# Kernel optimization log

Hardware: AMD Instinct MI355X
Metric: run time of the kernel (lower is better)

The kernel has to match this reference:

```python
import jax, jax.numpy as jnp
import numpy as np

B, T, D, H = 4, 2048, 2048, 16
DH = D // H

def setup_inputs() -> dict:
    key = jax.random.key(0)
    ks = jax.random.split(key, 9)
    s = 1.0 / np.sqrt(D)
    return {
        "x": jax.random.normal(ks[0], (B, T, D), dtype=jnp.float32),
        "Wq": jax.random.uniform(ks[1], (D, D), jnp.float32, -s, s),
        "bq": jax.random.uniform(ks[2], (D,), jnp.float32, -s, s),
        "Wk": jax.random.uniform(ks[3], (D, D), jnp.float32, -s, s),
        "bk": jax.random.uniform(ks[4], (D,), jnp.float32, -s, s),
        "Wv": jax.random.uniform(ks[5], (D, D), jnp.float32, -s, s),
        "bv": jax.random.uniform(ks[6], (D,), jnp.float32, -s, s),
        "Wo": jax.random.uniform(ks[7], (D, D), jnp.float32, -s, s),
        "bo": jax.random.uniform(ks[8], (D,), jnp.float32, -s, s),
    }

def reference(x, Wq, bq, Wk, bk, Wv, bv, Wo, bo):
    # projections: [B,T,D] -> [B,H,T,DH]
    def split_heads(y):
        return y.reshape(B, T, H, DH).transpose(0, 2, 1, 3)
    q = split_heads(x @ Wq + bq)
    k = split_heads(x @ Wk + bk)
    v = split_heads(x @ Wv + bv)
    scale = DH ** -0.5
    scores = jnp.einsum('bhtd,bhsd->bhts', q, k) * scale  # [B,H,T,T]
    causal = jnp.tril(jnp.ones((T, T), dtype=bool))
    scores = jnp.where(causal[None, None], scores, -jnp.inf)
    weights = jax.nn.softmax(scores, axis=-1)
    out = jnp.einsum('bhts,bhsd->bhtd', weights, v)  # [B,H,T,DH]
    out = out.transpose(0, 2, 1, 3).reshape(B, T, D)
    return out @ Wo + bo
```

## Files before the change

### kernel.cpp

```cpp
#include <hip/hip_runtime.h>
#include <hip/hip_bf16.h>

#define B_  4
#define T_  2048
#define D_  2048
#define H_  16
#define DH_ 128

typedef __attribute__((ext_vector_type(4))) float f32x4;
typedef __attribute__((ext_vector_type(8))) short short8;

__device__ __forceinline__ ushort f2bf(float f) {
    unsigned int u = __builtin_bit_cast(unsigned int, f);
    u += 0x7fffu + ((u >> 16) & 1u);
    return (ushort)(u >> 16);
}

__device__ __forceinline__ void glds16(const void* g, void* l) {
    __builtin_amdgcn_global_load_lds(
        (const __attribute__((address_space(1))) unsigned int*)g,
        (__attribute__((address_space(3))) unsigned int*)l, 16, 0, 0);
}

__global__ void cast_f32_bf16(const float* __restrict__ x, ushort* __restrict__ xb, int n) {
    int i = (blockIdx.x * 256 + threadIdx.x) * 4;
    if (i < n) {
        float4 v = *(const float4*)(x + i);
        ushort4 o;
        o.x = f2bf(v.x); o.y = f2bf(v.y); o.z = f2bf(v.z); o.w = f2bf(v.w);
        *(ushort4*)(xb + i) = o;
    }
}

__global__ void transpose_cast(const float* __restrict__ W, ushort* __restrict__ Wt) {
    __shared__ float tile[32][33];
    int tx = threadIdx.x, ty = threadIdx.y;
    int n0 = blockIdx.x * 32, k0 = blockIdx.y * 32;
#pragma unroll
    for (int i = 0; i < 4; i++)
        tile[ty + i * 8][tx] = W[(size_t)(k0 + ty + i * 8) * D_ + n0 + tx];
    __syncthreads();
#pragma unroll
    for (int i = 0; i < 4; i++)
        Wt[(size_t)(n0 + ty + i * 8) * D_ + k0 + tx] = f2bf(tile[tx][ty + i * 8]);
}

template <int MODE>
__global__ __launch_bounds__(256, 2) void gemm_bt(
    const ushort* __restrict__ A, const ushort* __restrict__ Bt,
    const float* __restrict__ bias, void* __restrict__ Cout,
    int M, int N, int K, float oscale)
{
    extern __shared__ char smem[];
    uint4* sA = (uint4*)smem;
    uint4* sB = (uint4*)(smem + 8192);

    const int tid  = threadIdx.x;
    const int row0 = blockIdx.y * 128, col0 = blockIdx.x * 128;

    const int mA = tid >> 2, g = tid & 3;
    const int gc = g ^ ((mA >> 2) & 3);
    const ushort* pa0 = A  + (size_t)(row0 + mA) * K + gc * 8;
    const ushort* pb0 = Bt + (size_t)(col0 + mA) * K + gc * 8;

    const int lane = tid & 63, w = tid >> 6;
    const int l15 = lane & 15, quad = lane >> 4;
    const int wm = w & 1, wn = w >> 1;
    const int csel = quad ^ ((l15 >> 2) & 3);
    int aoff[4], boff[4];
#pragma unroll
    for (int mt = 0; mt < 4; mt++) aoff[mt] = (wm * 64 + mt * 16 + l15) * 4 + csel;
#pragma unroll
    for (int nt = 0; nt < 4; nt++) boff[nt] = (wn * 64 + nt * 16 + l15) * 4 + csel;

    f32x4 acc[4][4] = {};

    const int kIter = K >> 5;
    for (int kt = 0; kt < kIter; ++kt) {
        if (kt) __syncthreads();
        glds16(pa0 + kt * 32,                     sA + tid);
        glds16(pa0 + kt * 32 + (size_t)64 * K,    sA + tid + 256);
        glds16(pb0 + kt * 32,                     sB + tid);
        glds16(pb0 + kt * 32 + (size_t)64 * K,    sB + tid + 256);
        __syncthreads();
        short8 af[4], bfr[4];
#pragma unroll
        for (int mt = 0; mt < 4; mt++) af[mt]  = __builtin_bit_cast(short8, sA[aoff[mt]]);
#pragma unroll
        for (int nt = 0; nt < 4; nt++) bfr[nt] = __builtin_bit_cast(short8, sB[boff[nt]]);
#pragma unroll
        for (int mt = 0; mt < 4; mt++)
#pragma unroll
            for (int nt = 0; nt < 4; nt++)
                acc[mt][nt] = __builtin_amdgcn_mfma_f32_16x16x32_bf16(af[mt], bfr[nt], acc[mt][nt], 0, 0, 0);
    }

    if constexpr (MODE == 0 || MODE == 1) {
#pragma unroll
        for (int nt = 0; nt < 4; nt++) {
            int col = col0 + wn * 64 + nt * 16 + l15;
            float bb = bias[col];
#pragma unroll
            for (int mt = 0; mt < 4; mt++) {
                int rowb = row0 + wm * 64 + mt * 16 + quad * 4;
#pragma unroll
                for (int r = 0; r < 4; r++) {
                    float v = (acc[mt][nt][r] + bb) * oscale;
                    if constexpr (MODE == 0)
                        ((ushort*)Cout)[(size_t)(rowb + r) * N + col] = f2bf(v);
                    else
                        ((float*)Cout)[(size_t)(rowb + r) * N + col] = v;
                }
            }
        }
    } else {
        __syncthreads();
        ushort* tr = (ushort*)smem;
#pragma unroll
        for (int nt = 0; nt < 4; nt++) {
            int cl = wn * 64 + nt * 16 + l15;
            float bb = bias[col0 + cl];
#pragma unroll
            for (int mt = 0; mt < 4; mt++) {
                int rl = wm * 64 + mt * 16 + quad * 4;
#pragma unroll
                for (int r = 0; r < 4; r++)
                    tr[cl * 136 + rl + r] = f2bf(acc[mt][nt][r] + bb);
            }
        }
        __syncthreads();
        ushort* C = (ushort*)Cout;
        int b = row0 >> 11, t0 = row0 & (T_ - 1), h = col0 >> 7;
        for (int idx = tid; idx < 2048; idx += 256) {
            int dh = idx >> 4, c = idx & 15;
            uint4 v = *(const uint4*)(tr + dh * 136 + c * 8);
            *(uint4*)(C + (size_t)((b * H_ + h) * DH_ + dh) * T_ + t0 + c * 8) = v;
        }
    }
}

__global__ __launch_bounds__(256, 4) void attn_kernel(
    const ushort* __restrict__ Q, const ushort* __restrict__ K,
    const ushort* __restrict__ Vt, ushort* __restrict__ O)
{
    __shared__ __align__(16) char smem[40960];
    uint4* kS = (uint4*)smem;
    uint4* vS = (uint4*)(smem + 16384);
    uint4* pS = (uint4*)(smem + 32768);

    const int tid = threadIdx.x;
    const int h = blockIdx.y, b = blockIdx.z;
    const int lane = tid & 63, w = tid >> 6, l15 = lane & 15, quad = lane >> 4;

    const int krow = tid >> 4;
    const int kchunk = (tid & 15) ^ (krow & 7);
    const ushort* kg = K + ((size_t)(b * T_) + krow) * D_ + h * DH_ + kchunk * 8;
    const int vrow = tid >> 3;
    const int vchunk = (tid & 7) ^ (vrow & 7);
    const ushort* vg = Vt + ((size_t)((b * H_ + h) * DH_) + vrow) * T_ + vchunk * 8;

    const int qts[2] = { (int)blockIdx.x, 31 - (int)blockIdx.x };

    for (int e = 0; e < 2; ++e) {
        const int qt = qts[e], q0 = qt * 64;

        short8 aq[4];
        {
            const ushort* qp = Q + ((size_t)(b * T_) + q0 + w * 16 + l15) * D_ + h * DH_ + quad * 8;
#pragma unroll
            for (int ks = 0; ks < 4; ++ks)
                aq[ks] = __builtin_bit_cast(short8, *(const uint4*)(qp + ks * 32));
        }

        f32x4 accO[8] = {};
        float mrow[4], lrow[4];
#pragma unroll
        for (int r = 0; r < 4; r++) { mrow[r] = -INFINITY; lrow[r] = 0.f; }

        for (int it = 0; it <= qt; ++it) {
            const int s0 = it * 64;
            __syncthreads();
            const ushort* kp = kg + (size_t)s0 * D_;
            const ushort* vp = vg + s0;
#pragma unroll
            for (int j = 0; j < 4; ++j) glds16(kp + (size_t)j * 16 * D_, kS + j * 256 + tid);
#pragma unroll
            for (int j = 0; j < 4; ++j) glds16(vp + (size_t)j * 32 * T_, vS + j * 256 + tid);
            __syncthreads();

            f32x4 s[4] = {};
#pragma unroll
            for (int ks = 0; ks < 4; ++ks)
#pragma unroll
                for (int nt = 0; nt < 4; ++nt) {
                    int n = nt * 16 + l15;
                    short8 bk = __builtin_bit_cast(short8, kS[n * 16 + ((ks * 4 + quad) ^ (n & 7))]);
                    s[nt] = __builtin_amdgcn_mfma_f32_16x16x32_bf16(aq[ks], bk, s[nt], 0, 0, 0);
                }

#pragma unroll
            for (int r = 0; r < 4; ++r) {
                const int qrow = q0 + w * 16 + quad * 4 + r;
                const int m = w * 16 + quad * 4 + r;
                float rmax = -INFINITY;
#pragma unroll
                for (int nt = 0; nt < 4; ++nt) {
                    float v = s[nt][r];
                    if (s0 + nt * 16 + l15 > qrow) v = -INFINITY;
                    s[nt][r] = v;
                    rmax = fmaxf(rmax, v);
                }
#pragma unroll
                for (int off = 1; off < 16; off <<= 1) rmax = fmaxf(rmax, __shfl_xor(rmax, off));
                float mnew  = fmaxf(mrow[r], rmax);
                float alpha = __expf(mrow[r] - mnew);
                mrow[r] = mnew;
                float sum = 0.f;
#pragma unroll
                for (int nt = 0; nt < 4; ++nt) {
                    float pv = __expf(s[nt][r] - mnew);
                    sum += pv;
                    int col = nt * 16 + l15;
                    ((ushort*)pS)[(m * 8 + ((col >> 3) ^ (m & 7))) * 8 + (col & 7)] = f2bf(pv);
                }
#pragma unroll
                for (int off = 1; off < 16; off <<= 1) sum += __shfl_xor(sum, off);
                lrow[r] = lrow[r] * alpha + sum;
#pragma unroll
                for (int nt = 0; nt < 8; ++nt) accO[nt][r] *= alpha;
            }

            const int mp = w * 16 + l15;
#pragma unroll
            for (int ks = 0; ks < 2; ++ks) {
                short8 ap = __builtin_bit_cast(short8, pS[mp * 8 + ((ks * 4 + quad) ^ (mp & 7))]);
#pragma unroll
                for (int nt = 0; nt < 8; ++nt) {
                    int n = nt * 16 + l15;
                    short8 bv = __builtin_bit_cast(short8, vS[n * 8 + ((ks * 4 + quad) ^ (n & 7))]);
                    accO[nt] = __builtin_amdgcn_mfma_f32_16x16x32_bf16(ap, bv, accO[nt], 0, 0, 0);
                }
            }
        }

#pragma unroll
        for (int nt = 0; nt < 8; ++nt) {
            int dh = nt * 16 + l15;
#pragma unroll
            for (int r = 0; r < 4; ++r) {
                int t = q0 + w * 16 + quad * 4 + r;
                O[((size_t)(b * T_ + t)) * D_ + h * DH_ + dh] = f2bf(accO[nt][r] / lrow[r]);
            }
        }
    }
}

extern "C" void kernel_launch(void* const* d_in, const int* in_sizes, int n_in,
                              void* d_out, int out_size, void* d_ws, size_t ws_size,
                              hipStream_t stream) {
    const float* x  = (const float*)d_in[0];
    const float* Wq = (const float*)d_in[1];
    const float* bq = (const float*)d_in[2];
    const float* Wk = (const float*)d_in[3];
    const float* bk = (const float*)d_in[4];
    const float* Wv = (const float*)d_in[5];
    const float* bv = (const float*)d_in[6];
    const float* Wo = (const float*)d_in[7];
    const float* bo = (const float*)d_in[8];

    char* ws = (char*)d_ws;
    const size_t MB = 1u << 20;
    ushort* xb  = (ushort*)(ws);
    ushort* Wqt = (ushort*)(ws + 32 * MB);
    ushort* Wkt = (ushort*)(ws + 40 * MB);
    ushort* Wvt = (ushort*)(ws + 48 * MB);
    ushort* Wot = (ushort*)(ws + 56 * MB);
    ushort* Qb  = (ushort*)(ws + 64 * MB);
    ushort* Kb  = (ushort*)(ws + 96 * MB);
    ushort* Vtb = (ushort*)(ws + 128 * MB);
    ushort* Ob  = (ushort*)(ws + 160 * MB);

    const int M = B_ * T_;
    const float qscale = 0.08838834764831845f;

    cast_f32_bf16<<<(M * D_) / 1024, 256, 0, stream>>>(x, xb, M * D_);
    dim3 tb(32, 8), tg(D_ / 32, D_ / 32);
    transpose_cast<<<tg, tb, 0, stream>>>(Wq, Wqt);
    transpose_cast<<<tg, tb, 0, stream>>>(Wk, Wkt);
    transpose_cast<<<tg, tb, 0, stream>>>(Wv, Wvt);
    transpose_cast<<<tg, tb, 0, stream>>>(Wo, Wot);

    dim3 gg(D_ / 128, M / 128);
    gemm_bt<0><<<gg, 256, 16384, stream>>>(xb, Wqt, bq, Qb,  M, D_, D_, qscale);
    gemm_bt<0><<<gg, 256, 16384, stream>>>(xb, Wkt, bk, Kb,  M, D_, D_, 1.0f);
    gemm_bt<2><<<gg, 256, 34816, stream>>>(xb, Wvt, bv, Vtb, M, D_, D_, 1.0f);

    attn_kernel<<<dim3(16, H_, B_), 256, 0, stream>>>(Qb, Kb, Vtb, Ob);

    gemm_bt<1><<<gg, 256, 16384, stream>>>(Ob, Wot, bo, (float*)d_out, M, D_, D_, 1.0f);
}
```

Baseline: 683.0 us.

## Keep attention probabilities in registers via transposed S and fp16 PV MFMA

Measured after the change: 635.5 us. -7.0%, faster.

```diff
diff --git a/kernel.cpp b/kernel.cpp
--- a/kernel.cpp
+++ b/kernel.cpp
@@ -9,11 +9,15 @@
 
 typedef __attribute__((ext_vector_type(4))) float f32x4;
 typedef __attribute__((ext_vector_type(8))) short short8;
+typedef __attribute__((ext_vector_type(4))) _Float16 half4;
 
 __device__ __forceinline__ ushort f2bf(float f) {
     unsigned int u = __builtin_bit_cast(unsigned int, f);
     u += 0x7fffu + ((u >> 16) & 1u);
     return (ushort)(u >> 16);
+}
+__device__ __forceinline__ ushort f2h(float f) {
+    return (ushort)(__builtin_bit_cast(unsigned int, __builtin_amdgcn_cvt_pkrtz(f, f)) & 0xffffu);
 }
 
 __device__ __forceinline__ void glds16(const void* g, void* l) {
@@ -125,7 +129,7 @@
                 int rl = wm * 64 + mt * 16 + quad * 4;
 #pragma unroll
                 for (int r = 0; r < 4; r++)
-                    tr[cl * 136 + rl + r] = f2bf(acc[mt][nt][r] + bb);
+                    tr[cl * 136 + rl + r] = f2h(acc[mt][nt][r] + bb);
             }
         }
         __syncthreads();
@@ -143,13 +147,17 @@
     const ushort* __restrict__ Q, const ushort* __restrict__ K,
     const ushort* __restrict__ Vt, ushort* __restrict__ O)
 {
-    __shared__ __align__(16) char smem[40960];
+    __shared__ __align__(16) char smem[32768];
     uint4* kS = (uint4*)smem;
     uint4* vS = (uint4*)(smem + 16384);
-    uint4* pS = (uint4*)(smem + 32768);
 
     const int tid = threadIdx.x;
-    const int h = blockIdx.y, b = blockIdx.z;
+    const int bid = blockIdx.x;
+    const int slot = bid >> 3;
+    const int g = (bid & 7) + 8 * (slot >> 4);
+    const int qx = slot & 15;
+    const int b = g >> 4, h = g & 15;
+
     const int lane = tid & 63, w = tid >> 6, l15 = lane & 15, quad = lane >> 4;
 
     const int krow = tid >> 4;
@@ -159,26 +167,26 @@
     const int vchunk = (tid & 7) ^ (vrow & 7);
     const ushort* vg = Vt + ((size_t)((b * H_ + h) * DH_) + vrow) * T_ + vchunk * 8;
 
-    const int qts[2] = { (int)blockIdx.x, 31 - (int)blockIdx.x };
+    const int qts[2] = { qx, 31 - qx };
 
     for (int e = 0; e < 2; ++e) {
         const int qt = qts[e], q0 = qt * 64;
+        const int qbase = q0 + w * 16;
 
         short8 aq[4];
         {
-            const ushort* qp = Q + ((size_t)(b * T_) + q0 + w * 16 + l15) * D_ + h * DH_ + quad * 8;
+            const ushort* qp = Q + ((size_t)(b * T_) + qbase + l15) * D_ + h * DH_ + quad * 8;
 #pragma unroll
             for (int ks = 0; ks < 4; ++ks)
                 aq[ks] = __builtin_bit_cast(short8, *(const uint4*)(qp + ks * 32));
         }
 
         f32x4 accO[8] = {};
-        float mrow[4], lrow[4];
-#pragma unroll
-        for (int r = 0; r < 4; r++) { mrow[r] = -INFINITY; lrow[r] = 0.f; }
+        float mrow = -INFINITY, lrow = 0.f;
 
         for (int it = 0; it <= qt; ++it) {
             const int s0 = it * 64;
+            const int stMax = (it == qt) ? (w + 1) : 4;
             __syncthreads();
             const ushort* kp = kg + (size_t)s0 * D_;
             const ushort* vp = vg + s0;
@@ -188,69 +196,91 @@
             for (int j = 0; j < 4; ++j) glds16(vp + (size_t)j * 32 * T_, vS + j * 256 + tid);
             __syncthreads();
 
-            f32x4 s[4] = {};
+            f32x4 sT[4] = {};
 #pragma unroll
             for (int ks = 0; ks < 4; ++ks)
 #pragma unroll
-                for (int nt = 0; nt < 4; ++nt) {
-                    int n = nt * 16 + l15;
-                    short8 bk = __builtin_bit_cast(short8, kS[n * 16 + ((ks * 4 + quad) ^ (n & 7))]);
-                    s[nt] = __builtin_amdgcn_mfma_f32_16x16x32_bf16(aq[ks], bk, s[nt], 0, 0, 0);
+                for (int st = 0; st < 4; ++st)
+                    if (st < stMax) {
+                        int row = st * 16 + l15;
+                        short8 ak = __builtin_bit_cast(short8, kS[row * 16 + ((ks * 4 + quad) ^ (row & 7))]);
+                        sT[st] = __builtin_amdgcn_mfma_f32_16x16x32_bf16(ak, aq[ks], sT[st], 0, 0, 0);
+                    }
+
+            if (s0 + 64 > qbase) {
+                const int q = qbase + l15;
+#pragma unroll
+                for (int st = 0; st < 4; ++st)
+                    if (st < stMax)
+#pragma unroll
+                        for (int r = 0; r < 4; ++r)
+                            if (s0 + st * 16 + quad * 4 + r > q) sT[st][r] = -INFINITY;
+            }
+
+            float rmax = -INFINITY;
+#pragma unroll
+            for (int st = 0; st < 4; ++st)
+                if (st < stMax)
+#pragma unroll
+                    for (int r = 0; r < 4; ++r) rmax = fmaxf(rmax, sT[st][r]);
+            rmax = fmaxf(rmax, __shfl_xor(rmax, 16));
+            rmax = fmaxf(rmax, __shfl_xor(rmax, 32));
+            float mnew  = fmaxf(mrow, rmax);
+            float alpha = __builtin_amdgcn_exp2f(mrow - mnew);
+            mrow = mnew;
+
+            float psum = 0.f;
+            half4 pb[4];
+#pragma unroll
+            for (int st = 0; st < 4; ++st)
+                if (st < stMax) {
+                    float p0 = __builtin_amdgcn_exp2f(sT[st][0] - mnew);
+                    float p1 = __builtin_amdgcn_exp2f(sT[st][1] - mnew);
+                    float p2 = __builtin_amdgcn_exp2f(sT[st][2] - mnew);
+                    float p3 = __builtin_amdgcn_exp2f(sT[st][3] - mnew);
+                    psum += (p0 + p1) + (p2 + p3);
+                    uint2 u;
+                    u.x = __builtin_bit_cast(unsigned int, __builtin_amdgcn_cvt_pkrtz(p0, p1));
+                    u.y = __builtin_bit_cast(unsigned int, __builtin_amdgcn_cvt_pkrtz(p2, p3));
+                    pb[st] = __builtin_bit_cast(half4, u);
                 }
-
-#pragma unroll
-            for (int r = 0; r < 4; ++r) {
-                const int qrow = q0 + w * 16 + quad * 4 + r;
-                const int m = w * 16 + quad * 4 + r;
-                float rmax = -INFINITY;
-#pragma unroll
-                for (int nt = 0; nt < 4; ++nt) {
-                    float v = s[nt][r];
-                    if (s0 + nt * 16 + l15 > qrow) v = -INFINITY;
-                    s[nt][r] = v;
-                    rmax = fmaxf(rmax, v);
+            psum += __shfl_xor(psum, 16);
+            psum += __shfl_xor(psum, 32);
+            lrow = lrow * alpha + psum;
+#pragma unroll
+            for (int nt = 0; nt < 8; ++nt)
+#pragma unroll
+                for (int r = 0; r < 4; ++r) accO[nt][r] *= alpha;
+
+            const ushort* vbase = (const ushort*)vS;
+#pragma unroll
+            for (int st = 0; st < 4; ++st)
+                if (st < stMax) {
+                    const int ch = (st * 2 + (quad >> 1));
+                    const int sub = (quad & 1) * 4;
+#pragma unroll
+                    for (int nt = 0; nt < 8; ++nt) {
+                        int dh = nt * 16 + l15;
+                        half4 vf = *(const half4*)(vbase + dh * 64 + ((ch ^ (l15 & 7)) * 8) + sub);
+                        accO[nt] = __builtin_amdgcn_mfma_f32_16x16x16f16(vf, pb[st], accO[nt], 0, 0, 0);
+                    }
                 }
-#pragma unroll
-                for (int off = 1; off < 16; off <<= 1) rmax = fmaxf(rmax, __shfl_xor(rmax, off));
-                float mnew  = fmaxf(mrow[r], rmax);
-                float alpha = __expf(mrow[r] - mnew);
-                mrow[r] = mnew;
-                float sum = 0.f;
-#pragma unroll
-                for (int nt = 0; nt < 4; ++nt) {
-                    float pv = __expf(s[nt][r] - mnew);
-                    sum += pv;
-                    int col = nt * 16 + l15;
-                    ((ushort*)pS)[(m * 8 + ((col >> 3) ^ (m & 7))) * 8 + (col & 7)] = f2bf(pv);
-                }
-#pragma unroll
-                for (int off = 1; off < 16; off <<= 1) sum += __shfl_xor(sum, off);
-                lrow[r] = lrow[r] * alpha + sum;
-#pragma unroll
-                for (int nt = 0; nt < 8; ++nt) accO[nt][r] *= alpha;
-            }
-
-            const int mp = w * 16 + l15;
-#pragma unroll
-            for (int ks = 0; ks < 2; ++ks) {
-                short8 ap = __builtin_bit_cast(short8, pS[mp * 8 + ((ks * 4 + quad) ^ (mp & 7))]);
-#pragma unroll
-                for (int nt = 0; nt < 8; ++nt) {
-                    int n = nt * 16 + l15;
-                    short8 bv = __builtin_bit_cast(short8, vS[n * 8 + ((ks * 4 + quad) ^ (n & 7))]);
-                    accO[nt] = __builtin_amdgcn_mfma_f32_16x16x32_bf16(ap, bv, accO[nt], 0, 0, 0);
-                }
-            }
-        }
-
+        }
+
+        __syncthreads();
+        ushort* eT = (ushort*)smem + w * 2176;
+        float inv = 1.0f / lrow;
 #pragma unroll
         for (int nt = 0; nt < 8; ++nt) {
-            int dh = nt * 16 + l15;
-#pragma unroll
-            for (int r = 0; r < 4; ++r) {
-                int t = q0 + w * 16 + quad * 4 + r;
-                O[((size_t)(b * T_ + t)) * D_ + h * DH_ + dh] = f2bf(accO[nt][r] / lrow[r]);
-            }
+            int dh = nt * 16 + quad * 4;
+#pragma unroll
+            for (int r = 0; r < 4; ++r)
+                eT[l15 * 136 + dh + r] = f2bf(accO[nt][r] * inv);
+        }
+        for (int idx = lane; idx < 256; idx += 64) {
+            int row = idx >> 4, c = idx & 15;
+            uint4 v = *(const uint4*)(eT + row * 136 + c * 8);
+            *(uint4*)(O + ((size_t)(b * T_) + q0 + w * 16 + row) * D_ + h * DH_ + c * 8) = v;
         }
     }
 }
@@ -281,7 +311,7 @@
     ushort* Ob  = (ushort*)(ws + 160 * MB);
 
     const int M = B_ * T_;
-    const float qscale = 0.08838834764831845f;
+    const float qscale = (float)(0.08838834764831845 * 1.4426950408889634);
 
     cast_f32_bf16<<<(M * D_) / 1024, 256, 0, stream>>>(x, xb, M * D_);
     dim3 tb(32, 8), tg(D_ / 32, D_ / 32);
@@ -295,7 +325,7 @@
     gemm_bt<0><<<gg, 256, 16384, stream>>>(xb, Wkt, bk, Kb,  M, D_, D_, 1.0f);
     gemm_bt<2><<<gg, 256, 34816, stream>>>(xb, Wvt, bv, Vtb, M, D_, D_, 1.0f);
 
-    attn_kernel<<<dim3(16, H_, B_), 256, 0, stream>>>(Qb, Kb, Vtb, Ob);
+    attn_kernel<<<dim3(1024), 256, 0, stream>>>(Qb, Kb, Vtb, Ob);
 
     gemm_bt<1><<<gg, 256, 16384, stream>>>(Ob, Wot, bo, (float*)d_out, M, D_, D_, 1.0f);
 }
```
